# Kernel tuning notes

Hardware: AMD Instinct MI355X
Metric: run time of the kernel (lower is better)

Reference implementation:

```python
import jax, jax.numpy as jnp
import numpy as np

K = 16          # neighbors per query (args.k)
EPS_NORM = 1e-5  # LayerNorm / BatchNorm eps (torch default)


def _knn_edges(xyz, B, n):
    # batch-aware kNN: equal-sized batches, edges never cross batch boundary
    x = xyz.reshape(B, n, 3)
    d2 = jnp.sum((x[:, :, None, :] - x[:, None, :, :]) ** 2, -1)   # [B,n,n]
    _, idx = jax.lax.top_k(-d2, K)                                 # [B,n,K] local neighbor ids
    col = (idx + (jnp.arange(B) * n)[:, None, None]).reshape(-1)   # source (neighbor) [E]
    row = jnp.repeat(jnp.arange(B * n), K)                         # target (query)    [E]
    return row, col


def _forward(support_xyz, batch_index, features, lang_features, mask_flattened,
             W1, b1, ln_g, ln_b, W2, b2,
             Wl1, bl1, bn_g, bn_b, Wl2, bl2,
             Wr1, br1, Wr2, br2, row, col):
    N = support_xyz.shape[0]
    B, L, Fl = lang_features.shape
    # feat_encoder: Linear -> LayerNorm -> ReLU -> Linear
    h = features @ W1 + b1
    mu = h.mean(-1, keepdims=True)
    var = ((h - mu) ** 2).mean(-1, keepdims=True)
    h = (h - mu) / jnp.sqrt(var + EPS_NORM) * ln_g + ln_b
    feats = jax.nn.relu(h) @ W2 + b2                               # [N,F]
    # lang_encoder: Linear -> BatchNorm1d (batch statistics) -> ReLU -> Linear
    hl = lang_features.reshape(B * L, Fl) @ Wl1 + bl1
    mul = hl.mean(0)
    varl = ((hl - mul) ** 2).mean(0)
    hl = (hl - mul) / jnp.sqrt(varl + EPS_NORM) * bn_g + bn_b
    lang = (jax.nn.relu(hl) @ Wl2 + bl2).reshape(B, L, -1)         # [B,L,F]
    lang_flat = lang[batch_index]                                  # [N,L,F]
    # per-point / per-token attention logits
    atten = jnp.einsum('nf,nlf->nl', feats, lang_flat)             # [N,L]
    # segment softmax over incoming kNN edges (CenterOp max / add)
    attenmax = jax.ops.segment_max(atten[col], row, num_segments=N, indices_are_sorted=True)
    a = jnp.exp(atten[col] - attenmax[row])                        # [E,L]
    attensum = jax.ops.segment_sum(a, row, num_segments=N, indices_are_sorted=True)
    # CenterConv message
    att = a / attensum[row] * mask_flattened[row]                  # [E,L]
    att = att / (att.sum(-1, keepdims=True) + 1e-7)
    ctx = jnp.einsum('el,elf->ef', att, lang_flat[col])            # [E,F] attended lang feat
    xi, xj = support_xyz[row], support_xyz[col]
    d = xi - xj
    nrm = jnp.sqrt(jnp.sum(d * d, -1, keepdims=True) + 1e-12)
    ew = jnp.concatenate([xi, xj, d, nrm], -1)                     # [E,10]
    ew = jax.nn.relu(ew @ Wr1 + br1) @ Wr2 + br2                   # [E,F] rel_encoder
    msg = feats[col] * ctx * ew                                    # [E,F]
    rel = jax.ops.segment_sum(msg, row, num_segments=N, indices_are_sorted=True)
    return feats + rel


def setup_inputs() -> dict:
    key = jax.random.key(0)
    ks = jax.random.split(key, 12)
    B, n, L = 4, 1024, 16
    N = B * n
    Fv, Fl, F = 256, 768, 128
    def w(k, shp, fan):
        return jax.random.normal(k, shp, jnp.float32) / np.sqrt(fan).astype(np.float32)
    mask = (jax.random.uniform(ks[3], (N, L)) < 0.8).astype(jnp.float32).at[:, 0].set(1.0)
    return {
        'support_xyz': jax.random.normal(ks[0], (N, 3), jnp.float32),
        'batch_index': jnp.repeat(jnp.arange(B), n),
        'features': jax.random.normal(ks[1], (N, Fv), jnp.float32),
        'lang_features': jax.random.normal(ks[2], (B, L, Fl), jnp.float32),
        'mask_flattened': mask,
        'W1': w(ks[4], (Fv, F), Fv), 'b1': jnp.zeros(F, jnp.float32),
        'ln_g': jnp.ones(F, jnp.float32), 'ln_b': jnp.zeros(F, jnp.float32),
        'W2': w(ks[5], (F, F), F), 'b2': jnp.zeros(F, jnp.float32),
        'Wl1': w(ks[6], (Fl, F), Fl), 'bl1': jnp.zeros(F, jnp.float32),
        'bn_g': jnp.ones(F, jnp.float32), 'bn_b': jnp.zeros(F, jnp.float32),
        'Wl2': w(ks[7], (F, F), F), 'bl2': jnp.zeros(F, jnp.float32),
        'Wr1': w(ks[8], (10, 64), 10), 'br1': jnp.zeros(64, jnp.float32),
        'Wr2': w(ks[9], (64, F), 64), 'br2': jnp.zeros(F, jnp.float32),
    }


def reference(support_xyz, batch_index, features, lang_features, mask_flattened,
              W1, b1, ln_g, ln_b, W2, b2,
              Wl1, bl1, bn_g, bn_b, Wl2, bl2,
              Wr1, br1, Wr2, br2):
    B = lang_features.shape[0]
    n = support_xyz.shape[0] // B
    row, col = _knn_edges(support_xyz, B, n)
    return _forward(support_xyz, batch_index, features, lang_features, mask_flattened,
                    W1, b1, ln_g, ln_b, W2, b2,
                    Wl1, bl1, bn_g, bn_b, Wl2, bl2,
                    Wr1, br1, Wr2, br2, row, col)
```

## Files before the change

### kernel.cpp

```cpp
#include <hip/hip_runtime.h>

typedef unsigned long long u64;
typedef short short8 __attribute__((ext_vector_type(8)));
typedef float f32x4 __attribute__((ext_vector_type(4)));

#define N_PTS   4096
#define B_SZ    4
#define N_PER_B 1024
#define L_TOK   16
#define FV      256
#define FL      768
#define FDIM    128
#define KNN     16
#define RH      64

__device__ __forceinline__ short f2bf(float f) {
    unsigned int x = __float_as_uint(f);
    unsigned int r = (x + 0x7fffu + ((x >> 16) & 1u)) >> 16;
    return (short)r;
}
__device__ __forceinline__ void fma4(float4& a, float s, const float4 w) {
    a.x += s * w.x; a.y += s * w.y; a.z += s * w.z; a.w += s * w.w;
}

__global__ __launch_bounds__(256) void kA_kernel(const float* __restrict__ xyz,
                                                 const float* __restrict__ lf,
                                                 const float* __restrict__ Wl1,
                                                 const float* __restrict__ bl1,
                                                 const float* __restrict__ Wr2,
                                                 int* __restrict__ knn,
                                                 float* __restrict__ hl,
                                                 short* __restrict__ wr2t) {
    __shared__ float smem[1024];
    int b = blockIdx.x, t = threadIdx.x;

    if (b < 1024) {
        int lane = t & 63;
        int q = b * 4 + (t >> 6);
        int base = (q >> 10) << 10;
        float qx = xyz[q * 3 + 0];
        float qy = xyz[q * 3 + 1];
        float qz = xyz[q * 3 + 2];
        u64 keys[16];
#pragma unroll
        for (int m = 0; m < 16; m++) {
            int j = base + lane + (m << 6);
            float dx = qx - xyz[j * 3 + 0];
            float dy = qy - xyz[j * 3 + 1];
            float dz = qz - xyz[j * 3 + 2];
            float d2 = __fadd_rn(__fadd_rn(__fmul_rn(dx, dx), __fmul_rn(dy, dy)),
                                 __fmul_rn(dz, dz));
            keys[m] = (((u64)__float_as_uint(d2)) << 32) | (unsigned int)j;
        }
        for (int r = 0; r < KNN; r++) {
            u64 lmin = keys[0];
#pragma unroll
            for (int m = 1; m < 16; m++) lmin = (keys[m] < lmin) ? keys[m] : lmin;
            u64 g = lmin;
#pragma unroll
            for (int off = 32; off > 0; off >>= 1) {
                u64 o = __shfl_xor(g, off, 64);
                g = (o < g) ? o : g;
            }
#pragma unroll
            for (int m = 0; m < 16; m++)
                if (keys[m] == g) keys[m] = ~0ULL;
            if (lane == 0) knn[q * KNN + r] = (int)(g & 0xffffffffu);
        }
    } else if (b < 1088) {
        int r = b - 1024;
        float* lrow = smem;
        float* part = smem + 768;
        for (int k = t; k < FL; k += 256) lrow[k] = lf[r * FL + k];
        __syncthreads();
        int c = t & 127, kh = t >> 7;
        float acc = (kh == 0) ? bl1[c] : 0.f;
        int k0 = kh * 384;
        for (int k = k0; k < k0 + 384; k++) acc += lrow[k] * Wl1[k * FDIM + c];
        part[kh * FDIM + c] = acc;
        __syncthreads();
        if (kh == 0) hl[r * FDIM + c] = part[c] + part[FDIM + c];
    } else {
        for (int p = t; p < RH * FDIM; p += 256) {
            int c = p >> 6, k = p & 63;
            wr2t[c * RH + k] = f2bf(Wr2[k * FDIM + c]);
        }
    }
}

__global__ __launch_bounds__(128) void lang2_kernel(const float* __restrict__ hl,
                                                    const float* __restrict__ bn_g,
                                                    const float* __restrict__ bn_b,
                                                    const float* __restrict__ Wl2,
                                                    const float* __restrict__ bl2,
                                                    float* __restrict__ lang,
                                                    short* __restrict__ langT) {
    __shared__ float rl4[4][FDIM];
    int t = threadIdx.x;
    int r0 = blockIdx.x * 4;
    float s = 0.f, s2 = 0.f;
    for (int r = 0; r < 64; r++) {
        float v = hl[r * FDIM + t];
        s += v; s2 += v * v;
    }
    float mu = s * (1.f / 64.f);
    float var = s2 * (1.f / 64.f) - mu * mu;
    float rs = rsqrtf(var + 1e-5f);
    float g = bn_g[t], bb = bn_b[t];
#pragma unroll
    for (int p = 0; p < 4; p++)
        rl4[p][t] = fmaxf((hl[(r0 + p) * FDIM + t] - mu) * rs * g + bb, 0.f);
    __syncthreads();
    float bv = bl2[t];
    float a[4] = {bv, bv, bv, bv};
    for (int k = 0; k < FDIM; k++) {
        float w = Wl2[k * FDIM + t];
        a[0] += rl4[0][k] * w;
        a[1] += rl4[1][k] * w;
        a[2] += rl4[2][k] * w;
        a[3] += rl4[3][k] * w;
    }
#pragma unroll
    for (int p = 0; p < 4; p++) {
        int r = r0 + p;
        lang[r * FDIM + t] = a[p];
        langT[((r >> 4) * FDIM + t) * L_TOK + (r & 15)] = f2bf(a[p]);
    }
}

__global__ __launch_bounds__(256) void feat_kernel(const float* __restrict__ features,
                                                   const float* __restrict__ W1,
                                                   const float* __restrict__ b1,
                                                   const float* __restrict__ ln_g,
                                                   const float* __restrict__ ln_b,
                                                   const float* __restrict__ W2,
                                                   const float* __restrict__ b2,
                                                   const float* __restrict__ lang,
                                                   float* __restrict__ feats,
                                                   float* __restrict__ atten) {
    __shared__ float fin[16 * FV];
    __shared__ float rbuf[16 * FDIM];
    __shared__ float fbuf[16 * FDIM];
    int t = threadIdx.x;
    int i0 = blockIdx.x * 16;
    {
        const float4* src = (const float4*)(features + i0 * FV);
        float4* dst = (float4*)fin;
#pragma unroll
        for (int v = 0; v < 4; v++) dst[t + 256 * v] = src[t + 256 * v];
    }
    __syncthreads();
    int cg = t & 31, ps = t >> 5;
    int c0 = cg * 4;
    int p0 = ps * 2, p1 = p0 + 1;

    float4 bv = *(const float4*)(b1 + c0);
    float4 a0 = bv, a1 = bv;
    for (int k4 = 0; k4 < FV / 4; k4++) {
        float4 f0 = *(const float4*)&fin[p0 * FV + k4 * 4];
        float4 f1 = *(const float4*)&fin[p1 * FV + k4 * 4];
        const float* wp = W1 + (k4 * 4) * FDIM + c0;
        float4 w;
        w = *(const float4*)(wp);            fma4(a0, f0.x, w); fma4(a1, f1.x, w);
        w = *(const float4*)(wp + FDIM);     fma4(a0, f0.y, w); fma4(a1, f1.y, w);
        w = *(const float4*)(wp + 2 * FDIM); fma4(a0, f0.z, w); fma4(a1, f1.z, w);
        w = *(const float4*)(wp + 3 * FDIM); fma4(a0, f0.w, w); fma4(a1, f1.w, w);
    }
    float s0 = a0.x + a0.y + a0.z + a0.w;
    float q0 = a0.x * a0.x + a0.y * a0.y + a0.z * a0.z + a0.w * a0.w;
    float s1 = a1.x + a1.y + a1.z + a1.w;
    float q1 = a1.x * a1.x + a1.y * a1.y + a1.z * a1.z + a1.w * a1.w;
#pragma unroll
    for (int off = 1; off < 32; off <<= 1) {
        s0 += __shfl_xor(s0, off, 32);
        q0 += __shfl_xor(q0, off, 32);
        s1 += __shfl_xor(s1, off, 32);
        q1 += __shfl_xor(q1, off, 32);
    }
    float mu0 = s0 * (1.f / 128.f), var0 = q0 * (1.f / 128.f) - mu0 * mu0;
    float mu1 = s1 * (1.f / 128.f), var1 = q1 * (1.f / 128.f) - mu1 * mu1;
    float rs0 = rsqrtf(var0 + 1e-5f), rs1 = rsqrtf(var1 + 1e-5f);
    float4 g4 = *(const float4*)(ln_g + c0);
    float4 lb4 = *(const float4*)(ln_b + c0);
    float4 r0v, r1v;
    r0v.x = fmaxf((a0.x - mu0) * rs0 * g4.x + lb4.x, 0.f);
    r0v.y = fmaxf((a0.y - mu0) * rs0 * g4.y + lb4.y, 0.f);
    r0v.z = fmaxf((a0.z - mu0) * rs0 * g4.z + lb4.z, 0.f);
    r0v.w = fmaxf((a0.w - mu0) * rs0 * g4.w + lb4.w, 0.f);
    r1v.x = fmaxf((a1.x - mu1) * rs1 * g4.x + lb4.x, 0.f);
    r1v.y = fmaxf((a1.y - mu1) * rs1 * g4.y + lb4.y, 0.f);
    r1v.z = fmaxf((a1.z - mu1) * rs1 * g4.z + lb4.z, 0.f);
    r1v.w = fmaxf((a1.w - mu1) * rs1 * g4.w + lb4.w, 0.f);
    *(float4*)&rbuf[p0 * FDIM + c0] = r0v;
    *(float4*)&rbuf[p1 * FDIM + c0] = r1v;
    __syncthreads();

    float4 bv2 = *(const float4*)(b2 + c0);
    float4 o0 = bv2, o1 = bv2;
    for (int k4 = 0; k4 < FDIM / 4; k4++) {
        float4 f0 = *(const float4*)&rbuf[p0 * FDIM + k4 * 4];
        float4 f1 = *(const float4*)&rbuf[p1 * FDIM + k4 * 4];
        const float* wp = W2 + (k4 * 4) * FDIM + c0;
        float4 w;
        w = *(const float4*)(wp);            fma4(o0, f0.x, w); fma4(o1, f1.x, w);
        w = *(const float4*)(wp + FDIM);     fma4(o0, f0.y, w); fma4(o1, f1.y, w);
        w = *(const float4*)(wp + 2 * FDIM); fma4(o0, f0.z, w); fma4(o1, f1.z, w);
        w = *(const float4*)(wp + 3 * FDIM); fma4(o0, f0.w, w); fma4(o1, f1.w, w);
    }
    *(float4*)(feats + (i0 + p0) * FDIM + c0) = o0;
    *(float4*)(feats + (i0 + p1) * FDIM + c0) = o1;
    *(float4*)&fbuf[p0 * FDIM + c0] = o0;
    *(float4*)&fbuf[p1 * FDIM + c0] = o1;
    __syncthreads();

    int p = t >> 4, l = t & 15;
    int bi = i0 >> 10;
    const float4* lr = (const float4*)(lang + (bi * L_TOK + l) * FDIM);
    const float4* fr = (const float4*)&fbuf[p * FDIM];
    float acc = 0.f;
#pragma unroll
    for (int k = 0; k < FDIM / 4; k++) {
        float4 x = lr[k], y = fr[k];
        acc += x.x * y.x + x.y * y.y + x.z * y.z + x.w * y.w;
    }
    atten[(i0 + p) * L_TOK + l] = acc;
}

__global__ __launch_bounds__(256) void edge_kernel(const float* __restrict__ xyz,
                                                   const float* __restrict__ mask,
                                                   const float* __restrict__ Wr1,
                                                   const float* __restrict__ br1,
                                                   const short* __restrict__ wr2t,
                                                   const float* __restrict__ br2,
                                                   const int* __restrict__ knn,
                                                   const short* __restrict__ langT,
                                                   const float* __restrict__ feats,
                                                   const float* __restrict__ atten,
                                                   float* __restrict__ out) {
    int lane = threadIdx.x & 63;
    int wid  = threadIdx.x >> 6;
    int i    = blockIdx.x * 4 + wid;
    int bi   = i >> 10;
    int quad = lane >> 4;
    int e16  = lane & 15;

    int idxe = knn[i * KNN + e16];

    float sat[8];
    if (quad < 2) {
        const float4* ap = (const float4*)(atten + idxe * L_TOK + quad * 8);
        float4 a0 = ap[0], a1 = ap[1];
        sat[0] = a0.x; sat[1] = a0.y; sat[2] = a0.z; sat[3] = a0.w;
        sat[4] = a1.x; sat[5] = a1.y; sat[6] = a1.z; sat[7] = a1.w;
    } else {
#pragma unroll
        for (int j = 0; j < 8; j++) sat[j] = 0.f;
    }

    float mx[8];
#pragma unroll
    for (int j = 0; j < 8; j++) mx[j] = sat[j];
#pragma unroll
    for (int off = 1; off < 16; off <<= 1) {
#pragma unroll
        for (int j = 0; j < 8; j++) mx[j] = fmaxf(mx[j], __shfl_xor(mx[j], off, 16));
    }
    float ex[8], sm[8];
#pragma unroll
    for (int j = 0; j < 8; j++) { ex[j] = __expf(sat[j] - mx[j]); sm[j] = ex[j]; }
#pragma unroll
    for (int off = 1; off < 16; off <<= 1) {
#pragma unroll
        for (int j = 0; j < 8; j++) sm[j] += __shfl_xor(sm[j], off, 16);
    }
    float st[8];
    if (quad < 2) {
        const float4* mp = (const float4*)(mask + i * L_TOK + quad * 8);
        float4 m0 = mp[0], m1 = mp[1];
        float mv[8] = {m0.x, m0.y, m0.z, m0.w, m1.x, m1.y, m1.z, m1.w};
#pragma unroll
        for (int j = 0; j < 8; j++) st[j] = ex[j] * (mv[j] / sm[j]);
    } else {
#pragma unroll
        for (int j = 0; j < 8; j++) st[j] = 0.f;
    }
    float s = st[0] + st[1] + st[2] + st[3] + st[4] + st[5] + st[6] + st[7];
    s += __shfl_xor(s, 16, 64);
    s += __shfl_xor(s, 32, 64);
    float inv2 = 1.f / (s + 1e-7f);
    short8 sattA;
#pragma unroll
    for (int j = 0; j < 8; j++) sattA[j] = f2bf(st[j] * inv2);

    float xi0 = xyz[i * 3 + 0], xi1 = xyz[i * 3 + 1], xi2 = xyz[i * 3 + 2];
    float xj0 = xyz[idxe * 3 + 0], xj1 = xyz[idxe * 3 + 1], xj2 = xyz[idxe * 3 + 2];
    float d0 = xi0 - xj0, d1 = xi1 - xj1, d2v = xi2 - xj2;
    float nr = sqrtf(d0 * d0 + d1 * d1 + d2v * d2v + 1e-12f);
    float ein[10] = {xi0, xi1, xi2, xj0, xj1, xj2, d0, d1, d2v, nr};
    short8 hidA[2];
#pragma unroll
    for (int sstep = 0; sstep < 2; sstep++) {
        int k0 = sstep * 32 + quad * 8;
        float h[8];
        const float4* bp = (const float4*)(br1 + k0);
        float4 b0 = bp[0], b1v = bp[1];
        h[0] = b0.x; h[1] = b0.y; h[2] = b0.z; h[3] = b0.w;
        h[4] = b1v.x; h[5] = b1v.y; h[6] = b1v.z; h[7] = b1v.w;
#pragma unroll
        for (int m = 0; m < 10; m++) {
            const float4* wp = (const float4*)(Wr1 + m * RH + k0);
            float4 w0 = wp[0], w1 = wp[1];
            float em = ein[m];
            h[0] += em * w0.x; h[1] += em * w0.y; h[2] += em * w0.z; h[3] += em * w0.w;
            h[4] += em * w1.x; h[5] += em * w1.y; h[6] += em * w1.z; h[7] += em * w1.w;
        }
#pragma unroll
        for (int j = 0; j < 8; j++) hidA[sstep][j] = f2bf(fmaxf(h[j], 0.f));
    }

    int idxr[4];
#pragma unroll
    for (int r = 0; r < 4; r++) idxr[r] = knn[i * KNN + quad * 4 + r];

#pragma unroll 2
    for (int tile = 0; tile < 8; tile++) {
        int cc = tile * 16 + e16;
        const short8* w2p = (const short8*)(wr2t + cc * RH);
        f32x4 accew = {0.f, 0.f, 0.f, 0.f};
        accew = __builtin_amdgcn_mfma_f32_16x16x32_bf16(hidA[0], w2p[quad],     accew, 0, 0, 0);
        accew = __builtin_amdgcn_mfma_f32_16x16x32_bf16(hidA[1], w2p[4 + quad], accew, 0, 0, 0);
        short8 lsB;
        if (quad < 2) {
            lsB = ((const short8*)(langT + (bi * FDIM + cc) * L_TOK))[quad];
        } else {
#pragma unroll
            for (int j = 0; j < 8; j++) lsB[j] = 0;
        }
        f32x4 accctx = {0.f, 0.f, 0.f, 0.f};
        accctx = __builtin_amdgcn_mfma_f32_16x16x32_bf16(sattA, lsB, accctx, 0, 0, 0);

        float br2c = br2[cc];
        float msum = 0.f;
#pragma unroll
        for (int r = 0; r < 4; r++) {
            float fj = feats[idxr[r] * FDIM + cc];
            msum += fj * accctx[r] * (accew[r] + br2c);
        }
        msum += __shfl_xor(msum, 16, 64);
        msum += __shfl_xor(msum, 32, 64);
        if (lane < 16)
            out[i * FDIM + cc] = feats[i * FDIM + cc] + msum;
    }
}

extern "C" void kernel_launch(void* const* d_in, const int* in_sizes, int n_in,
                              void* d_out, int out_size, void* d_ws, size_t ws_size,
                              hipStream_t stream) {
    const float* xyz   = (const float*)d_in[0];
    const float* features = (const float*)d_in[2];
    const float* lang_f   = (const float*)d_in[3];
    const float* mask     = (const float*)d_in[4];
    const float* W1   = (const float*)d_in[5];
    const float* b1   = (const float*)d_in[6];
    const float* ln_g = (const float*)d_in[7];
    const float* ln_b = (const float*)d_in[8];
    const float* W2   = (const float*)d_in[9];
    const float* b2   = (const float*)d_in[10];
    const float* Wl1  = (const float*)d_in[11];
    const float* bl1  = (const float*)d_in[12];
    const float* bn_g = (const float*)d_in[13];
    const float* bn_b = (const float*)d_in[14];
    const float* Wl2  = (const float*)d_in[15];
    const float* bl2  = (const float*)d_in[16];
    const float* Wr1  = (const float*)d_in[17];
    const float* br1  = (const float*)d_in[18];
    const float* Wr2  = (const float*)d_in[19];
    const float* br2  = (const float*)d_in[20];

    float* ws_feats = (float*)d_ws;
    float* ws_atten = ws_feats + N_PTS * FDIM;
    float* ws_lang  = ws_atten + N_PTS * L_TOK;
    float* ws_hl    = ws_lang + B_SZ * L_TOK * FDIM;
    int*   ws_knn   = (int*)(ws_hl + 64 * FDIM);
    short* ws_wr2t  = (short*)(ws_knn + N_PTS * KNN);
    short* ws_langT = ws_wr2t + FDIM * RH;

    kA_kernel<<<1089, 256, 0, stream>>>(xyz, lang_f, Wl1, bl1, Wr2,
                                        ws_knn, ws_hl, ws_wr2t);
    lang2_kernel<<<16, 128, 0, stream>>>(ws_hl, bn_g, bn_b, Wl2, bl2,
                                         ws_lang, ws_langT);
    feat_kernel<<<N_PTS / 16, 256, 0, stream>>>(features, W1, b1, ln_g, ln_b, W2, b2,
                                                ws_lang, ws_feats, ws_atten);
    edge_kernel<<<N_PTS / 4, 256, 0, stream>>>(xyz, mask, Wr1, br1, ws_wr2t, br2,
                                               ws_knn, ws_langT, ws_feats, ws_atten,
                                               (float*)d_out);
}
```

Baseline: 174.2 us.

## Move feature encoder GEMMs to split-bf16 MFMA with pre-transposed weights

The feature encoder's two matmuls (256->128 and 128->128) now run on MFMA 16x16x32 bf16 instructions instead of scalar FP32 FMAs. Activations and weights are split into bf16 hi and lo parts, and three MFMAs per tile keep close to FP32 accuracy. The weights are transposed and split once in extra blocks of the first kernel. LayerNorm statistics are reduced across waves through shared memory, and the shared buffers are padded against bank conflicts. A few loops in the other kernels also get unroll pragmas. The trade-off is more setup work, extra workspace and a small loss of precision versus pure FP32.

```diff
diff --git a/kernel.cpp b/kernel.cpp
--- a/kernel.cpp
+++ b/kernel.cpp
@@ -2,6 +2,7 @@
 
 typedef unsigned long long u64;
 typedef short short8 __attribute__((ext_vector_type(8)));
+typedef short short4v __attribute__((ext_vector_type(4)));
 typedef float f32x4 __attribute__((ext_vector_type(4)));
 
 #define N_PTS   4096
@@ -14,13 +15,17 @@
 #define KNN     16
 #define RH      64
 
+#define FINS 264
+#define RBS  136
+#define FBS  132
+
 __device__ __forceinline__ short f2bf(float f) {
     unsigned int x = __float_as_uint(f);
     unsigned int r = (x + 0x7fffu + ((x >> 16) & 1u)) >> 16;
     return (short)r;
 }
-__device__ __forceinline__ void fma4(float4& a, float s, const float4 w) {
-    a.x += s * w.x; a.y += s * w.y; a.z += s * w.z; a.w += s * w.w;
+__device__ __forceinline__ float bf2f(short s) {
+    return __uint_as_float(((unsigned int)(unsigned short)s) << 16);
 }
 
 __global__ __launch_bounds__(256) void kA_kernel(const float* __restrict__ xyz,
@@ -28,9 +33,15 @@
                                                  const float* __restrict__ Wl1,
                                                  const float* __restrict__ bl1,
                                                  const float* __restrict__ Wr2,
+                                                 const float* __restrict__ W1,
+                                                 const float* __restrict__ W2,
                                                  int* __restrict__ knn,
                                                  float* __restrict__ hl,
-                                                 short* __restrict__ wr2t) {
+                                                 short* __restrict__ wr2t,
+                                                 short* __restrict__ w1t_hi,
+                                                 short* __restrict__ w1t_lo,
+                                                 short* __restrict__ w2t_hi,
+                                                 short* __restrict__ w2t_lo) {
     __shared__ float smem[1024];
     int b = blockIdx.x, t = threadIdx.x;
 
@@ -76,14 +87,32 @@
         int c = t & 127, kh = t >> 7;
         float acc = (kh == 0) ? bl1[c] : 0.f;
         int k0 = kh * 384;
+#pragma unroll 8
         for (int k = k0; k < k0 + 384; k++) acc += lrow[k] * Wl1[k * FDIM + c];
         part[kh * FDIM + c] = acc;
         __syncthreads();
         if (kh == 0) hl[r * FDIM + c] = part[c] + part[FDIM + c];
-    } else {
+    } else if (b == 1088) {
         for (int p = t; p < RH * FDIM; p += 256) {
             int c = p >> 6, k = p & 63;
             wr2t[c * RH + k] = f2bf(Wr2[k * FDIM + c]);
+        }
+    } else if (b == 1089) {
+        for (int p = t; p < FDIM * FDIM; p += 256) {
+            int k = p >> 7, c = p & 127;
+            float v = W2[p];
+            short h = f2bf(v);
+            w2t_hi[c * FDIM + k] = h;
+            w2t_lo[c * FDIM + k] = f2bf(v - bf2f(h));
+        }
+    } else {
+        int kbase = (b - 1090) * 128;
+        for (int p = t; p < 128 * FDIM; p += 256) {
+            int k = kbase + (p >> 7), c = p & 127;
+            float v = W1[k * FDIM + c];
+            short h = f2bf(v);
+            w1t_hi[c * FV + k] = h;
+            w1t_lo[c * FV + k] = f2bf(v - bf2f(h));
         }
     }
 }
@@ -99,6 +128,7 @@
     int t = threadIdx.x;
     int r0 = blockIdx.x * 4;
     float s = 0.f, s2 = 0.f;
+#pragma unroll 8
     for (int r = 0; r < 64; r++) {
         float v = hl[r * FDIM + t];
         s += v; s2 += v * v;
@@ -113,6 +143,7 @@
     __syncthreads();
     float bv = bl2[t];
     float a[4] = {bv, bv, bv, bv};
+#pragma unroll 8
     for (int k = 0; k < FDIM; k++) {
         float w = Wl2[k * FDIM + t];
         a[0] += rl4[0][k] * w;
@@ -129,101 +160,144 @@
 }
 
 __global__ __launch_bounds__(256) void feat_kernel(const float* __restrict__ features,
-                                                   const float* __restrict__ W1,
                                                    const float* __restrict__ b1,
                                                    const float* __restrict__ ln_g,
                                                    const float* __restrict__ ln_b,
-                                                   const float* __restrict__ W2,
                                                    const float* __restrict__ b2,
+                                                   const short* __restrict__ w1t_hi,
+                                                   const short* __restrict__ w1t_lo,
+                                                   const short* __restrict__ w2t_hi,
+                                                   const short* __restrict__ w2t_lo,
                                                    const float* __restrict__ lang,
                                                    float* __restrict__ feats,
                                                    float* __restrict__ atten) {
-    __shared__ float fin[16 * FV];
-    __shared__ float rbuf[16 * FDIM];
-    __shared__ float fbuf[16 * FDIM];
+    __shared__ short fin_hi[16 * FINS], fin_lo[16 * FINS];
+    __shared__ short rb_hi[16 * RBS], rb_lo[16 * RBS];
+    __shared__ float fbuf[16 * FBS];
+    __shared__ float red_s[4 * 16], red_q[4 * 16];
     int t = threadIdx.x;
+    int w = t >> 6, lane = t & 63, quad = lane >> 4, e16 = lane & 15;
     int i0 = blockIdx.x * 16;
+
     {
         const float4* src = (const float4*)(features + i0 * FV);
-        float4* dst = (float4*)fin;
-#pragma unroll
-        for (int v = 0; v < 4; v++) dst[t + 256 * v] = src[t + 256 * v];
+#pragma unroll
+        for (int v = 0; v < 4; v++) {
+            int flat = t + 256 * v;
+            float4 x = src[flat];
+            int p = flat >> 6, k = (flat & 63) * 4;
+            short4v hi, lo;
+            hi[0] = f2bf(x.x); lo[0] = f2bf(x.x - bf2f(hi[0]));
+            hi[1] = f2bf(x.y); lo[1] = f2bf(x.y - bf2f(hi[1]));
+            hi[2] = f2bf(x.z); lo[2] = f2bf(x.z - bf2f(hi[2]));
+            hi[3] = f2bf(x.w); lo[3] = f2bf(x.w - bf2f(hi[3]));
+            *(short4v*)&fin_hi[p * FINS + k] = hi;
+            *(short4v*)&fin_lo[p * FINS + k] = lo;
+        }
     }
     __syncthreads();
-    int cg = t & 31, ps = t >> 5;
-    int c0 = cg * 4;
-    int p0 = ps * 2, p1 = p0 + 1;
-
-    float4 bv = *(const float4*)(b1 + c0);
-    float4 a0 = bv, a1 = bv;
-    for (int k4 = 0; k4 < FV / 4; k4++) {
-        float4 f0 = *(const float4*)&fin[p0 * FV + k4 * 4];
-        float4 f1 = *(const float4*)&fin[p1 * FV + k4 * 4];
-        const float* wp = W1 + (k4 * 4) * FDIM + c0;
-        float4 w;
-        w = *(const float4*)(wp);            fma4(a0, f0.x, w); fma4(a1, f1.x, w);
-        w = *(const float4*)(wp + FDIM);     fma4(a0, f0.y, w); fma4(a1, f1.y, w);
-        w = *(const float4*)(wp + 2 * FDIM); fma4(a0, f0.z, w); fma4(a1, f1.z, w);
-        w = *(const float4*)(wp + 3 * FDIM); fma4(a0, f0.w, w); fma4(a1, f1.w, w);
-    }
-    float s0 = a0.x + a0.y + a0.z + a0.w;
-    float q0 = a0.x * a0.x + a0.y * a0.y + a0.z * a0.z + a0.w * a0.w;
-    float s1 = a1.x + a1.y + a1.z + a1.w;
-    float q1 = a1.x * a1.x + a1.y * a1.y + a1.z * a1.z + a1.w * a1.w;
-#pragma unroll
-    for (int off = 1; off < 32; off <<= 1) {
-        s0 += __shfl_xor(s0, off, 32);
-        q0 += __shfl_xor(q0, off, 32);
-        s1 += __shfl_xor(s1, off, 32);
-        q1 += __shfl_xor(q1, off, 32);
-    }
-    float mu0 = s0 * (1.f / 128.f), var0 = q0 * (1.f / 128.f) - mu0 * mu0;
-    float mu1 = s1 * (1.f / 128.f), var1 = q1 * (1.f / 128.f) - mu1 * mu1;
-    float rs0 = rsqrtf(var0 + 1e-5f), rs1 = rsqrtf(var1 + 1e-5f);
-    float4 g4 = *(const float4*)(ln_g + c0);
-    float4 lb4 = *(const float4*)(ln_b + c0);
-    float4 r0v, r1v;
-    r0v.x = fmaxf((a0.x - mu0) * rs0 * g4.x + lb4.x, 0.f);
-    r0v.y = fmaxf((a0.y - mu0) * rs0 * g4.y + lb4.y, 0.f);
-    r0v.z = fmaxf((a0.z - mu0) * rs0 * g4.z + lb4.z, 0.f);
-    r0v.w = fmaxf((a0.w - mu0) * rs0 * g4.w + lb4.w, 0.f);
-    r1v.x = fmaxf((a1.x - mu1) * rs1 * g4.x + lb4.x, 0.f);
-    r1v.y = fmaxf((a1.y - mu1) * rs1 * g4.y + lb4.y, 0.f);
-    r1v.z = fmaxf((a1.z - mu1) * rs1 * g4.z + lb4.z, 0.f);
-    r1v.w = fmaxf((a1.w - mu1) * rs1 * g4.w + lb4.w, 0.f);
-    *(float4*)&rbuf[p0 * FDIM + c0] = r0v;
-    *(float4*)&rbuf[p1 * FDIM + c0] = r1v;
+
+    int c0 = 32 * w + e16, c1 = c0 + 16;
+
+    f32x4 acc0 = {0.f, 0.f, 0.f, 0.f}, acc1 = {0.f, 0.f, 0.f, 0.f};
+#pragma unroll
+    for (int s = 0; s < 8; s++) {
+        int ko = s * 32 + quad * 8;
+        short8 Ah = *(const short8*)&fin_hi[e16 * FINS + ko];
+        short8 Al = *(const short8*)&fin_lo[e16 * FINS + ko];
+        short8 B0h = *(const short8*)&w1t_hi[c0 * FV + ko];
+        short8 B0l = *(const short8*)&w1t_lo[c0 * FV + ko];
+        short8 B1h = *(const short8*)&w1t_hi[c1 * FV + ko];
+        short8 B1l = *(const short8*)&w1t_lo[c1 * FV + ko];
+        acc0 = __builtin_amdgcn_mfma_f32_16x16x32_bf16(Ah, B0h, acc0, 0, 0, 0);
+        acc0 = __builtin_amdgcn_mfma_f32_16x16x32_bf16(Ah, B0l, acc0, 0, 0, 0);
+        acc0 = __builtin_amdgcn_mfma_f32_16x16x32_bf16(Al, B0h, acc0, 0, 0, 0);
+        acc1 = __builtin_amdgcn_mfma_f32_16x16x32_bf16(Ah, B1h, acc1, 0, 0, 0);
+        acc1 = __builtin_amdgcn_mfma_f32_16x16x32_bf16(Ah, B1l, acc1, 0, 0, 0);
+        acc1 = __builtin_amdgcn_mfma_f32_16x16x32_bf16(Al, B1h, acc1, 0, 0, 0);
+    }
+    float b1c0 = b1[c0], b1c1 = b1[c1];
+    float h0[4], h1[4], sp[4], qp[4];
+#pragma unroll
+    for (int r = 0; r < 4; r++) {
+        h0[r] = acc0[r] + b1c0;
+        h1[r] = acc1[r] + b1c1;
+        sp[r] = h0[r] + h1[r];
+        qp[r] = h0[r] * h0[r] + h1[r] * h1[r];
+    }
+#pragma unroll
+    for (int off = 1; off < 16; off <<= 1) {
+#pragma unroll
+        for (int r = 0; r < 4; r++) {
+            sp[r] += __shfl_xor(sp[r], off, 16);
+            qp[r] += __shfl_xor(qp[r], off, 16);
+        }
+    }
+    if (e16 == 0) {
+#pragma unroll
+        for (int r = 0; r < 4; r++) {
+            red_s[w * 16 + quad * 4 + r] = sp[r];
+            red_q[w * 16 + quad * 4 + r] = qp[r];
+        }
+    }
     __syncthreads();
-
-    float4 bv2 = *(const float4*)(b2 + c0);
-    float4 o0 = bv2, o1 = bv2;
-    for (int k4 = 0; k4 < FDIM / 4; k4++) {
-        float4 f0 = *(const float4*)&rbuf[p0 * FDIM + k4 * 4];
-        float4 f1 = *(const float4*)&rbuf[p1 * FDIM + k4 * 4];
-        const float* wp = W2 + (k4 * 4) * FDIM + c0;
-        float4 w;
-        w = *(const float4*)(wp);            fma4(o0, f0.x, w); fma4(o1, f1.x, w);
-        w = *(const float4*)(wp + FDIM);     fma4(o0, f0.y, w); fma4(o1, f1.y, w);
-        w = *(const float4*)(wp + 2 * FDIM); fma4(o0, f0.z, w); fma4(o1, f1.z, w);
-        w = *(const float4*)(wp + 3 * FDIM); fma4(o0, f0.w, w); fma4(o1, f1.w, w);
-    }
-    *(float4*)(feats + (i0 + p0) * FDIM + c0) = o0;
-    *(float4*)(feats + (i0 + p1) * FDIM + c0) = o1;
-    *(float4*)&fbuf[p0 * FDIM + c0] = o0;
-    *(float4*)&fbuf[p1 * FDIM + c0] = o1;
+    float g0 = ln_g[c0], g1 = ln_g[c1], be0 = ln_b[c0], be1 = ln_b[c1];
+#pragma unroll
+    for (int r = 0; r < 4; r++) {
+        int p = quad * 4 + r;
+        float S = red_s[p] + red_s[16 + p] + red_s[32 + p] + red_s[48 + p];
+        float Q = red_q[p] + red_q[16 + p] + red_q[32 + p] + red_q[48 + p];
+        float mu = S * (1.f / 128.f);
+        float var = Q * (1.f / 128.f) - mu * mu;
+        float rs = rsqrtf(var + 1e-5f);
+        float r0 = fmaxf((h0[r] - mu) * rs * g0 + be0, 0.f);
+        float r1 = fmaxf((h1[r] - mu) * rs * g1 + be1, 0.f);
+        short hh;
+        hh = f2bf(r0); rb_hi[p * RBS + c0] = hh; rb_lo[p * RBS + c0] = f2bf(r0 - bf2f(hh));
+        hh = f2bf(r1); rb_hi[p * RBS + c1] = hh; rb_lo[p * RBS + c1] = f2bf(r1 - bf2f(hh));
+    }
     __syncthreads();
 
-    int p = t >> 4, l = t & 15;
+    f32x4 o0 = {0.f, 0.f, 0.f, 0.f}, o1 = {0.f, 0.f, 0.f, 0.f};
+#pragma unroll
+    for (int s = 0; s < 4; s++) {
+        int ko = s * 32 + quad * 8;
+        short8 Ah = *(const short8*)&rb_hi[e16 * RBS + ko];
+        short8 Al = *(const short8*)&rb_lo[e16 * RBS + ko];
+        short8 B0h = *(const short8*)&w2t_hi[c0 * FDIM + ko];
+        short8 B0l = *(const short8*)&w2t_lo[c0 * FDIM + ko];
+        short8 B1h = *(const short8*)&w2t_hi[c1 * FDIM + ko];
+        short8 B1l = *(const short8*)&w2t_lo[c1 * FDIM + ko];
+        o0 = __builtin_amdgcn_mfma_f32_16x16x32_bf16(Ah, B0h, o0, 0, 0, 0);
+        o0 = __builtin_amdgcn_mfma_f32_16x16x32_bf16(Ah, B0l, o0, 0, 0, 0);
+        o0 = __builtin_amdgcn_mfma_f32_16x16x32_bf16(Al, B0h, o0, 0, 0, 0);
+        o1 = __builtin_amdgcn_mfma_f32_16x16x32_bf16(Ah, B1h, o1, 0, 0, 0);
+        o1 = __builtin_amdgcn_mfma_f32_16x16x32_bf16(Ah, B1l, o1, 0, 0, 0);
+        o1 = __builtin_amdgcn_mfma_f32_16x16x32_bf16(Al, B1h, o1, 0, 0, 0);
+    }
+    float b20 = b2[c0], b21 = b2[c1];
+#pragma unroll
+    for (int r = 0; r < 4; r++) {
+        int p = quad * 4 + r;
+        float f0 = o0[r] + b20, f1 = o1[r] + b21;
+        feats[(i0 + p) * FDIM + c0] = f0;
+        feats[(i0 + p) * FDIM + c1] = f1;
+        fbuf[p * FBS + c0] = f0;
+        fbuf[p * FBS + c1] = f1;
+    }
+    __syncthreads();
+
+    int pp = t >> 4, l = t & 15;
     int bi = i0 >> 10;
     const float4* lr = (const float4*)(lang + (bi * L_TOK + l) * FDIM);
-    const float4* fr = (const float4*)&fbuf[p * FDIM];
     float acc = 0.f;
 #pragma unroll
     for (int k = 0; k < FDIM / 4; k++) {
-        float4 x = lr[k], y = fr[k];
+        float4 x = lr[k];
+        float4 y = *(const float4*)&fbuf[pp * FBS + 4 * k];
         acc += x.x * y.x + x.y * y.y + x.z * y.z + x.w * y.w;
     }
-    atten[(i0 + p) * L_TOK + l] = acc;
+    atten[(i0 + pp) * L_TOK + l] = acc;
 }
 
 __global__ __launch_bounds__(256) void edge_kernel(const float* __restrict__ xyz,
@@ -384,12 +458,19 @@
     int*   ws_knn   = (int*)(ws_hl + 64 * FDIM);
     short* ws_wr2t  = (short*)(ws_knn + N_PTS * KNN);
     short* ws_langT = ws_wr2t + FDIM * RH;
-
-    kA_kernel<<<1089, 256, 0, stream>>>(xyz, lang_f, Wl1, bl1, Wr2,
-                                        ws_knn, ws_hl, ws_wr2t);
+    short* ws_w1t_hi = ws_langT + B_SZ * FDIM * L_TOK;
+    short* ws_w1t_lo = ws_w1t_hi + FDIM * FV;
+    short* ws_w2t_hi = ws_w1t_lo + FDIM * FV;
+    short* ws_w2t_lo = ws_w2t_hi + FDIM * FDIM;
+
+    kA_kernel<<<1092, 256, 0, stream>>>(xyz, lang_f, Wl1, bl1, Wr2, W1, W2,
+                                        ws_knn, ws_hl, ws_wr2t,
+                                        ws_w1t_hi, ws_w1t_lo, ws_w2t_hi, ws_w2t_lo);
     lang2_kernel<<<16, 128, 0, stream>>>(ws_hl, bn_g, bn_b, Wl2, bl2,
                                          ws_lang, ws_langT);
-    feat_kernel<<<N_PTS / 16, 256, 0, stream>>>(features, W1, b1, ln_g, ln_b, W2, b2,
+    feat_kernel<<<N_PTS / 16, 256, 0, stream>>>(features, b1, ln_g, ln_b, b2,
+                                                ws_w1t_hi, ws_w1t_lo,
+                                                ws_w2t_hi, ws_w2t_lo,
                                                 ws_lang, ws_feats, ws_atten);
     edge_kernel<<<N_PTS / 4, 256, 0, stream>>>(xyz, mask, Wr1, br1, ws_wr2t, br2,
                                                ws_knn, ws_langT, ws_feats, ws_atten,
```

Result: no change. 174.1 us (-0.0%).
